# Kernel optimization log

Hardware: AMD Instinct MI355X
Metric: run time of the kernel (lower is better)

## Reference

```python
import jax, jax.numpy as jnp
import numpy as np

# Config constants (match init_kwargs)
D_MODEL = 1024
N_EXPERTS = 8
EXPERT_SCALE = 2          # experts per base group -> n_base_groups = 4
N_FEAT = 16
BANK_DIM = 32
RAW_FEAT = N_FEAT * BANK_DIM   # 512
PROJ_DIM = 256
R_HIDDEN = 256
E_HIDDEN = 256
TOP_K = 2
TEMP = 1.0
LN_EPS = 1e-5


def _layernorm(x, g, b):
    mu = jnp.mean(x, axis=-1, keepdims=True)
    var = jnp.mean((x - mu) ** 2, axis=-1, keepdims=True)
    return (x - mu) * jax.lax.rsqrt(var + LN_EPS) * g + b


def _softmax_top_k(logits, k):
    # keep top-k logits, mask rest to -inf, softmax
    topv = jax.lax.top_k(logits, k)[0]
    thresh = topv[..., -1:]
    masked = jnp.where(logits >= thresh, logits, -jnp.inf)
    return jax.nn.softmax(masked, axis=-1)


def setup_inputs() -> dict:
    key = jax.random.key(0)
    ks = jax.random.split(key, 24)
    B, S = 4, 2048
    s = 0.02
    inp = {
        "hidden": jax.random.normal(ks[0], (B, S, D_MODEL), jnp.float32),
        "feat": jax.random.normal(ks[1], (B, S, N_FEAT), jnp.float32),
        "feat_bank": jax.random.normal(ks[2], (B, S, N_FEAT, BANK_DIM), jnp.float32),
        "item_seq_len": jax.random.randint(ks[3], (B,), 1, S + 1, jnp.int64),
        # pre-LN
        "ln_g": jnp.ones((D_MODEL,), jnp.float32),
        "ln_b": jnp.zeros((D_MODEL,), jnp.float32),
        # router feature projector (2 layers: Linear -> GELU -> Linear)
        "fp_w1": jax.random.normal(ks[4], (RAW_FEAT, PROJ_DIM), jnp.float32) * s,
        "fp_b1": jnp.zeros((PROJ_DIM,), jnp.float32),
        "fp_w2": jax.random.normal(ks[5], (PROJ_DIM, PROJ_DIM), jnp.float32) * s,
        "fp_b2": jnp.zeros((PROJ_DIM,), jnp.float32),
        # learned router MLP: d_in = d_model + proj_dim
        "r_w1": jax.random.normal(ks[6], (D_MODEL + PROJ_DIM, R_HIDDEN), jnp.float32) * s,
        "r_b1": jnp.zeros((R_HIDDEN,), jnp.float32),
        "r_w2": jax.random.normal(ks[7], (R_HIDDEN, N_EXPERTS), jnp.float32) * s,
        "r_b2": jnp.zeros((N_EXPERTS,), jnp.float32),
        # rule router (linear on raw stage features)
        "rr_w": jax.random.normal(ks[8], (N_FEAT, N_EXPERTS), jnp.float32) * s,
        "rr_b": jnp.zeros((N_EXPERTS,), jnp.float32),
        # per-expert FFN
        "e_w1": jax.random.normal(ks[9], (N_EXPERTS, D_MODEL, E_HIDDEN), jnp.float32) * s,
        "e_b1": jnp.zeros((N_EXPERTS, E_HIDDEN), jnp.float32),
        "e_w2": jax.random.normal(ks[10], (N_EXPERTS, E_HIDDEN, D_MODEL), jnp.float32) * s,
        "e_b2": jnp.zeros((N_EXPERTS, D_MODEL), jnp.float32),
        "alpha": jnp.ones((), jnp.float32),
    }
    return inp


def reference(hidden, feat, feat_bank, item_seq_len, ln_g, ln_b,
              fp_w1, fp_b1, fp_w2, fp_b2,
              r_w1, r_b1, r_w2, r_b2,
              rr_w, rr_b,
              e_w1, e_b1, e_w2, e_b2, alpha):
    B, S, D = hidden.shape
    h_norm = _layernorm(hidden, ln_g, ln_b)  # [B,S,D]

    # router feature path: flatten bank, 2-layer GELU projector
    bank_flat = feat_bank.reshape(B, S, RAW_FEAT)
    proj = jnp.dot(jax.nn.gelu(jnp.dot(bank_flat, fp_w1) + fp_b1), fp_w2) + fp_b2  # [B,S,P]

    # token-mode router input: concat hidden + projected features
    router_input = jnp.concatenate([h_norm, proj], axis=-1)
    rule_logits = jnp.dot(feat, rr_w) + rr_b  # rule router on raw stage features

    raw_logits = jnp.dot(jax.nn.gelu(jnp.dot(router_input, r_w1) + r_b1), r_w2) + r_b2
    scaled_logits = raw_logits / max(TEMP, 1e-6)
    gate_weights = _softmax_top_k(scaled_logits, TOP_K)           # [B,S,E]
    rule_target_logits = rule_logits / max(TEMP, 1e-6)

    # expert group: per-expert 2-layer GELU FFN on h_norm
    h1 = jax.nn.gelu(jnp.einsum('bsd,edh->bseh', h_norm, e_w1) + e_b1)
    expert_out = jnp.einsum('bseh,ehd->bsed', h1, e_w2) + e_b2    # [B,S,E,D]

    stage_out = jnp.einsum('bse,bsed->bsd', gate_weights, expert_out)
    next_hidden = hidden + alpha * stage_out

    # _aggregate_group_weights: expert_group_idx = arange(E)//EXPERT_SCALE is
    # contiguous, so gather+sum per group == reshape+sum over the scale axis
    n_groups = N_EXPERTS // EXPERT_SCALE
    group_weights = gate_weights.reshape(B, S, n_groups, EXPERT_SCALE).sum(-1)

    return (next_hidden, stage_out, gate_weights, scaled_logits, group_weights, rule_target_logits)
```

## Files before the change

### kernel.cpp

```cpp
#include <hip/hip_runtime.h>
#include <stdint.h>


typedef unsigned short u16;
using bf16x8 = __attribute__((ext_vector_type(8))) short;
using f32x4  = __attribute__((ext_vector_type(4))) float;

__device__ __forceinline__ float gelu_tanh(float x) {
  float x3 = x * x * x;
  float t = tanhf(0.7978845608028654f * (x + 0.044715f * x3));
  return 0.5f * x * (1.0f + t);
}

__device__ __forceinline__ u16 f2bf(float f) {
  uint32_t u = __float_as_uint(f);
  u = u + 0x7fffu + ((u >> 16) & 1u);
  return (u16)(u >> 16);
}
__device__ __forceinline__ float b2f(u16 h) {
  return __uint_as_float(((uint32_t)h) << 16);
}

__device__ __forceinline__ void gll16(const void* g, void* l) {
  __builtin_amdgcn_global_load_lds(
      (const __attribute__((address_space(1))) void*)g,
      (__attribute__((address_space(3))) void*)l, 16, 0, 0);
}

__global__ __launch_bounds__(256) void split_bank_kernel(const float* __restrict__ x,
    u16* __restrict__ hi, u16* __restrict__ lo) {
  int i4 = blockIdx.x * 256 + threadIdx.x;
  float4 v = ((const float4*)x)[i4];
  ushort4 h, l;
  h.x = f2bf(v.x); l.x = f2bf(v.x - b2f(h.x));
  h.y = f2bf(v.y); l.y = f2bf(v.y - b2f(h.y));
  h.z = f2bf(v.z); l.z = f2bf(v.z - b2f(h.z));
  h.w = f2bf(v.w); l.w = f2bf(v.w - b2f(h.w));
  ((ushort4*)hi)[i4] = h;
  ((ushort4*)lo)[i4] = l;
}

__global__ __launch_bounds__(256) void prep_w_kernel(
    const float* __restrict__ fp_w1, const float* __restrict__ fp_w2,
    const float* __restrict__ r_w1, const float* __restrict__ e_w2,
    u16* __restrict__ w1h, u16* __restrict__ w1l,
    u16* __restrict__ w2h, u16* __restrict__ w2l,
    u16* __restrict__ rwh, u16* __restrict__ rwl,
    u16* __restrict__ ew2t) {
  int idx = blockIdx.x * 256 + threadIdx.x;
  if (idx < 131072) {
    int n = idx >> 9, k = idx & 511;
    float v = fp_w1[k * 256 + n];
    u16 h = f2bf(v); w1h[idx] = h; w1l[idx] = f2bf(v - b2f(h));
  } else if (idx < 196608) {
    int j = idx - 131072;
    int n = j >> 8, k = j & 255;
    float v = fp_w2[k * 256 + n];
    u16 h = f2bf(v); w2h[j] = h; w2l[j] = f2bf(v - b2f(h));
  } else if (idx < 524288) {
    int j = idx - 196608;
    int n = j / 1280, k = j - n * 1280;
    float v = r_w1[k * 256 + n];
    u16 h = f2bf(v); rwh[j] = h; rwl[j] = f2bf(v - b2f(h));
  } else {
    int j = idx - 524288;
    int d = j >> 11, q = j & 2047;
    ew2t[j] = f2bf(e_w2[q * 1024 + d]);
  }
}

__global__ __launch_bounds__(256) void prep_w1t_kernel(const float* __restrict__ ew1,
                                                       u16* __restrict__ w1t) {
  int idx = blockIdx.x * 256 + threadIdx.x;
  int k = idx & 1023, n = idx >> 10;
  int e = n >> 8, h = n & 255;
  w1t[idx] = f2bf(ew1[(e << 18) + (k << 8) + h]);
}

__global__ __launch_bounds__(256) void ln_kernel(const float* __restrict__ hidden,
    const float* __restrict__ ln_g, const float* __restrict__ ln_b,
    const float* __restrict__ feat, const float* __restrict__ rr_w,
    const float* __restrict__ rr_b,
    u16* __restrict__ h_hi, u16* __restrict__ h_lo, float* __restrict__ rule) {
  int t = blockIdx.x;
  int tid = threadIdx.x;
  float4 v = ((const float4*)(hidden + (size_t)t * 1024))[tid];
  float s = v.x + v.y + v.z + v.w;
#pragma unroll
  for (int o = 32; o > 0; o >>= 1) s += __shfl_down(s, o);
  __shared__ float red[4];
  __shared__ float stats[2];
  int wid = tid >> 6, lane = tid & 63;
  if (lane == 0) red[wid] = s;
  __syncthreads();
  if (tid == 0) stats[0] = (red[0] + red[1] + red[2] + red[3]) * (1.0f / 1024.0f);
  __syncthreads();
  float mu = stats[0];
  float dx = v.x - mu, dy = v.y - mu, dz = v.z - mu, dw = v.w - mu;
  float q = dx * dx + dy * dy + dz * dz + dw * dw;
#pragma unroll
  for (int o = 32; o > 0; o >>= 1) q += __shfl_down(q, o);
  if (lane == 0) red[wid] = q;
  __syncthreads();
  if (tid == 0) {
    float var = (red[0] + red[1] + red[2] + red[3]) * (1.0f / 1024.0f) + 1e-5f;
    float r = rsqrtf(var);
    r = r * (1.5f - 0.5f * var * r * r);
    stats[1] = r;
  }
  __syncthreads();
  float r = stats[1];
  float4 g = ((const float4*)ln_g)[tid];
  float4 b = ((const float4*)ln_b)[tid];
  float4 o;
  o.x = dx * r * g.x + b.x;
  o.y = dy * r * g.y + b.y;
  o.z = dz * r * g.z + b.z;
  o.w = dw * r * g.w + b.w;
  ushort4 hv, lv;
  hv.x = f2bf(o.x); lv.x = f2bf(o.x - b2f(hv.x));
  hv.y = f2bf(o.y); lv.y = f2bf(o.y - b2f(hv.y));
  hv.z = f2bf(o.z); lv.z = f2bf(o.z - b2f(hv.z));
  hv.w = f2bf(o.w); lv.w = f2bf(o.w - b2f(hv.w));
  ((ushort4*)(h_hi + (size_t)t * 1024))[tid] = hv;
  ((ushort4*)(h_lo + (size_t)t * 1024))[tid] = lv;
  if (tid < 8) {
    float acc = rr_b[tid];
#pragma unroll
    for (int f = 0; f < 16; f++) acc += feat[t * 16 + f] * rr_w[f * 8 + tid];
    rule[t * 8 + tid] = acc;
  }
}

__global__ __launch_bounds__(256) void gemm3_kernel(
    const u16* __restrict__ Ah, const u16* __restrict__ Al, int lda,
    int kchunk, int nz1,
    const u16* __restrict__ A2h, const u16* __restrict__ A2l, int lda2,
    int klen2, int bkoff2,
    const u16* __restrict__ Bth, const u16* __restrict__ Btl, int Kb,
    float* __restrict__ parts) {
  __shared__ u16 Ash[128 * 32];
  __shared__ u16 Asl[128 * 32];
  __shared__ u16 Bsh[128 * 32];
  __shared__ u16 Bsl[128 * 32];
  int tid = threadIdx.x;
  int z = blockIdx.z;
  const u16 *pAh, *pAl;
  int lda_, akoff, bkoff, klen;
  if (z < nz1) {
    pAh = Ah; pAl = Al; lda_ = lda; akoff = z * kchunk; bkoff = akoff; klen = kchunk;
  } else {
    pAh = A2h; pAl = A2l; lda_ = lda2; akoff = 0; bkoff = bkoff2; klen = klen2;
  }
  int row0 = blockIdx.y * 128, col0 = blockIdx.x * 128;
  int wave = tid >> 6, lane = tid & 63;
  int wr = (wave >> 1) * 64, wc = (wave & 1) * 64;
  int l16 = lane & 15, qd = lane >> 4;
  f32x4 acc[4][4];
#pragma unroll
  for (int i = 0; i < 4; i++)
#pragma unroll
    for (int j = 0; j < 4; j++) acc[i][j] = 0.0f;

  int r0 = tid >> 2, kc = tid & 3;
  const u16* gAh0 = pAh + (size_t)(row0 + r0) * lda_ + akoff + kc * 8;
  const u16* gAh1 = gAh0 + (size_t)64 * lda_;
  const u16* gAl0 = pAl + (size_t)(row0 + r0) * lda_ + akoff + kc * 8;
  const u16* gAl1 = gAl0 + (size_t)64 * lda_;
  const u16* gBh0 = Bth + (size_t)(col0 + r0) * Kb + bkoff + kc * 8;
  const u16* gBh1 = gBh0 + (size_t)64 * Kb;
  const u16* gBl0 = Btl + (size_t)(col0 + r0) * Kb + bkoff + kc * 8;
  const u16* gBl1 = gBl0 + (size_t)64 * Kb;
  u16* dAh = Ash + tid * 8;
  u16* dAl = Asl + tid * 8;
  u16* dBh = Bsh + tid * 8;
  u16* dBl = Bsl + tid * 8;

  for (int k0 = 0; k0 < klen; k0 += 32) {
    __syncthreads();
    gll16(gAh0 + k0, dAh);
    gll16(gAh1 + k0, dAh + 2048);
    gll16(gAl0 + k0, dAl);
    gll16(gAl1 + k0, dAl + 2048);
    gll16(gBh0 + k0, dBh);
    gll16(gBh1 + k0, dBh + 2048);
    gll16(gBl0 + k0, dBl);
    gll16(gBl1 + k0, dBl + 2048);
    __syncthreads();
    bf16x8 afh[4], afl[4], bfh[4], bfl[4];
#pragma unroll
    for (int i = 0; i < 4; i++) {
      afh[i] = *((const bf16x8*)(Ash + (wr + i * 16 + l16) * 32 + qd * 8));
      afl[i] = *((const bf16x8*)(Asl + (wr + i * 16 + l16) * 32 + qd * 8));
      bfh[i] = *((const bf16x8*)(Bsh + (wc + i * 16 + l16) * 32 + qd * 8));
      bfl[i] = *((const bf16x8*)(Bsl + (wc + i * 16 + l16) * 32 + qd * 8));
    }
#pragma unroll
    for (int i = 0; i < 4; i++)
#pragma unroll
      for (int j = 0; j < 4; j++) {
        acc[i][j] = __builtin_amdgcn_mfma_f32_16x16x32_bf16(afh[i], bfh[j], acc[i][j], 0, 0, 0);
        acc[i][j] = __builtin_amdgcn_mfma_f32_16x16x32_bf16(afl[i], bfh[j], acc[i][j], 0, 0, 0);
        acc[i][j] = __builtin_amdgcn_mfma_f32_16x16x32_bf16(afh[i], bfl[j], acc[i][j], 0, 0, 0);
      }
  }

  float* pz = parts + (size_t)z * 2097152;
#pragma unroll
  for (int i = 0; i < 4; i++)
#pragma unroll
    for (int j = 0; j < 4; j++) {
      int cl = wc + j * 16 + l16;
#pragma unroll
      for (int rr = 0; rr < 4; rr++) {
        int rl = wr + i * 16 + qd * 4 + rr;
        pz[(size_t)(row0 + rl) * 256 + col0 + cl] = acc[i][j][rr];
      }
    }
}

__global__ __launch_bounds__(256) void epi_bf_kernel(const float* __restrict__ parts,
    int nz, const float* __restrict__ bias, int do_gelu,
    u16* __restrict__ hi, u16* __restrict__ lo) {
  int i4 = blockIdx.x * 256 + threadIdx.x;
  float4 s = ((const float4*)parts)[i4];
  for (int zz = 1; zz < nz; zz++) {
    float4 p = ((const float4*)parts)[(size_t)zz * 524288 + i4];
    s.x += p.x; s.y += p.y; s.z += p.z; s.w += p.w;
  }
  float4 bv = ((const float4*)bias)[i4 & 63];
  s.x += bv.x; s.y += bv.y; s.z += bv.z; s.w += bv.w;
  if (do_gelu) {
    s.x = gelu_tanh(s.x); s.y = gelu_tanh(s.y);
    s.z = gelu_tanh(s.z); s.w = gelu_tanh(s.w);
  }
  ushort4 h, l;
  h.x = f2bf(s.x); l.x = f2bf(s.x - b2f(h.x));
  h.y = f2bf(s.y); l.y = f2bf(s.y - b2f(h.y));
  h.z = f2bf(s.z); l.z = f2bf(s.z - b2f(h.z));
  h.w = f2bf(s.w); l.w = f2bf(s.w - b2f(h.w));
  ((ushort4*)hi)[i4] = h;
  ((ushort4*)lo)[i4] = l;
}

__global__ __launch_bounds__(256) void epi_f32_kernel(const float* __restrict__ parts,
    int nz, const float* __restrict__ bias, float* __restrict__ out) {
  int i4 = blockIdx.x * 256 + threadIdx.x;
  float4 s = ((const float4*)parts)[i4];
  for (int zz = 1; zz < nz; zz++) {
    float4 p = ((const float4*)parts)[(size_t)zz * 524288 + i4];
    s.x += p.x; s.y += p.y; s.z += p.z; s.w += p.w;
  }
  float4 bv = ((const float4*)bias)[i4 & 63];
  s.x = gelu_tanh(s.x + bv.x);
  s.y = gelu_tanh(s.y + bv.y);
  s.z = gelu_tanh(s.z + bv.z);
  s.w = gelu_tanh(s.w + bv.w);
  ((float4*)out)[i4] = s;
}

__global__ __launch_bounds__(256) void gate_kernel(const float* __restrict__ r1,
    const float* __restrict__ r_w2, const float* __restrict__ r_b2,
    float* __restrict__ gates, float* __restrict__ slog, float* __restrict__ gw) {
  __shared__ float w2s[2048];
  __shared__ float r1s[32][260];
  __shared__ float lg[32][8];
  int tid = threadIdx.x;
  int t0 = blockIdx.x * 32;
  for (int i = tid; i < 2048; i += 256) w2s[i] = r_w2[i];
  for (int i = tid; i < 32 * 256; i += 256) {
    int tt = i >> 8, k = i & 255;
    r1s[tt][k] = r1[(size_t)(t0 + tt) * 256 + k];
  }
  __syncthreads();
  int tl = tid >> 3, e = tid & 7;
  float acc = r_b2[e];
  for (int k = 0; k < 256; k++) acc += r1s[tl][k] * w2s[k * 8 + e];
  lg[tl][e] = acc;
  __syncthreads();
  if (tid < 32) {
    int t = t0 + tid;
    float l[8];
#pragma unroll
    for (int i = 0; i < 8; i++) l[i] = lg[tid][i];
    float m1 = -1e30f, m2 = -1e30f;
#pragma unroll
    for (int i = 0; i < 8; i++) {
      float v = l[i];
      if (v > m1) { m2 = m1; m1 = v; }
      else if (v > m2) m2 = v;
    }
    float w[8];
    float se = 0.0f;
#pragma unroll
    for (int i = 0; i < 8; i++) {
      float ex = (l[i] >= m2) ? expf(l[i] - m1) : 0.0f;
      w[i] = ex;
      se += ex;
    }
    float inv = 1.0f / se;
#pragma unroll
    for (int i = 0; i < 8; i++) {
      gates[(size_t)t * 8 + i] = w[i] * inv;
      slog[(size_t)t * 8 + i] = l[i];
    }
#pragma unroll
    for (int gi = 0; gi < 4; gi++)
      gw[(size_t)t * 4 + gi] = (w[2 * gi] + w[2 * gi + 1]) * inv;
  }
}

template <int MODE>
__global__ __launch_bounds__(256) void mfma_gemm(const u16* __restrict__ A,
    const u16* __restrict__ Bt, int N, int K,
    const float* __restrict__ bias, const float* __restrict__ gates,
    u16* __restrict__ outb, const float* __restrict__ hidden,
    const float* __restrict__ alpha_p, float* __restrict__ stage,
    float* __restrict__ next) {
  __shared__ u16 As[128 * 32];
  __shared__ u16 Bs[128 * 32];
  __shared__ float gs[128 * 8];
  __shared__ float b2s[8 * 128];
  int tid = threadIdx.x;
  int row0 = blockIdx.y * 128, col0 = blockIdx.x * 128;
  int wave = tid >> 6, lane = tid & 63;
  int wr = (wave >> 1) * 64, wc = (wave & 1) * 64;
  int l16 = lane & 15, qd = lane >> 4;
  f32x4 acc[4][4];
#pragma unroll
  for (int i = 0; i < 4; i++)
#pragma unroll
    for (int j = 0; j < 4; j++) acc[i][j] = 0.0f;

  int r0 = tid >> 2, kc = tid & 3;
  const u16* Ap0 = A + (size_t)(row0 + r0) * K + kc * 8;
  const u16* Ap1 = Ap0 + (size_t)64 * K;
  const u16* Bp0 = Bt + (size_t)(col0 + r0) * K + kc * 8;
  const u16* Bp1 = Bp0 + (size_t)64 * K;
  u16* dA = As + tid * 8;
  u16* dB = Bs + tid * 8;

  for (int k0 = 0; k0 < K; k0 += 32) {
    __syncthreads();
    gll16(Ap0 + k0, dA);
    gll16(Ap1 + k0, dA + 2048);
    gll16(Bp0 + k0, dB);
    gll16(Bp1 + k0, dB + 2048);
    __syncthreads();
    bf16x8 af[4], bfr[4];
#pragma unroll
    for (int i = 0; i < 4; i++) {
      af[i]  = *((const bf16x8*)(As + (wr + i * 16 + l16) * 32 + qd * 8));
      bfr[i] = *((const bf16x8*)(Bs + (wc + i * 16 + l16) * 32 + qd * 8));
    }
#pragma unroll
    for (int i = 0; i < 4; i++)
#pragma unroll
      for (int j = 0; j < 4; j++)
        acc[i][j] = __builtin_amdgcn_mfma_f32_16x16x32_bf16(af[i], bfr[j], acc[i][j], 0, 0, 0);
  }

  for (int i = tid; i < 1024; i += 256)
    gs[i] = gates[(size_t)(row0 + (i >> 3)) * 8 + (i & 7)];
  if (MODE == 1) {
    for (int i = tid; i < 1024; i += 256)
      b2s[i] = bias[(size_t)(i >> 7) * 1024 + col0 + (i & 127)];
  }
  __syncthreads();

  if (MODE == 0) {
#pragma unroll
    for (int i = 0; i < 4; i++) {
#pragma unroll
      for (int j = 0; j < 4; j++) {
        int cl = wc + j * 16 + l16;
        int col = col0 + cl;
        float bcol = bias[col];
        int e = col >> 8;
#pragma unroll
        for (int rr = 0; rr < 4; rr++) {
          int rl = wr + i * 16 + qd * 4 + rr;
          int row = row0 + rl;
          float v = acc[i][j][rr] + bcol;
          v = gelu_tanh(v) * gs[rl * 8 + e];
          outb[(size_t)row * N + col] = f2bf(v);
        }
      }
    }
  } else {
    float al = alpha_p[0];
#pragma unroll
    for (int i = 0; i < 4; i++) {
#pragma unroll
      for (int j = 0; j < 4; j++) {
        int cl = wc + j * 16 + l16;
        int col = col0 + cl;
#pragma unroll
        for (int rr = 0; rr < 4; rr++) {
          int rl = wr + i * 16 + qd * 4 + rr;
          int row = row0 + rl;
          float sb = 0.0f;
#pragma unroll
          for (int e = 0; e < 8; e++) sb += gs[rl * 8 + e] * b2s[e * 128 + cl];
          float v = acc[i][j][rr] + sb;
          size_t o = (size_t)row * N + col;
          stage[o] = v;
          next[o] = hidden[o] + al * v;
        }
      }
    }
  }
}

extern "C" void kernel_launch(void* const* d_in, const int* in_sizes, int n_in,
                              void* d_out, int out_size, void* d_ws, size_t ws_size,
                              hipStream_t stream) {
  const float* hidden    = (const float*)d_in[0];
  const float* feat      = (const float*)d_in[1];
  const float* feat_bank = (const float*)d_in[2];
  const float* ln_g  = (const float*)d_in[4];
  const float* ln_b  = (const float*)d_in[5];
  const float* fp_w1 = (const float*)d_in[6];
  const float* fp_b1 = (const float*)d_in[7];
  const float* fp_w2 = (const float*)d_in[8];
  const float* fp_b2 = (const float*)d_in[9];
  const float* r_w1  = (const float*)d_in[10];
  const float* r_b1  = (const float*)d_in[11];
  const float* r_w2  = (const float*)d_in[12];
  const float* r_b2  = (const float*)d_in[13];
  const float* rr_w  = (const float*)d_in[14];
  const float* rr_b  = (const float*)d_in[15];
  const float* e_w1  = (const float*)d_in[16];
  const float* e_b1  = (const float*)d_in[17];
  const float* e_w2  = (const float*)d_in[18];
  const float* e_b2  = (const float*)d_in[19];
  const float* alpha = (const float*)d_in[20];

  char* ob = (char*)d_out;
  float* next  = (float*)ob;
  float* stage = (float*)(ob + 33554432);
  float* gates = (float*)(ob + 67108864);
  float* slog  = gates + 65536;
  float* gw    = slog + 65536;
  float* rule  = gw + 32768;

  u16* bank_hi  = (u16*)(ob);
  u16* bank_lo  = (u16*)(ob + 8388608);
  u16* fpw1t_hi = (u16*)(ob + 16777216);
  u16* fpw1t_lo = (u16*)(ob + 17039360);
  u16* mid_hi   = (u16*)(ob + 16777216);
  u16* mid_lo   = (u16*)(ob + 20971520);
  u16* fpw2t_hi = (u16*)(ob + 25165824);
  u16* fpw2t_lo = (u16*)(ob + 25296896);
  u16* proj_hi  = (u16*)(ob + 25165824);
  u16* proj_lo  = (u16*)(ob + 29360128);
  u16* w1t      = (u16*)(ob);
  char* sb = ob + 33554432;
  float* parts  = (float*)sb;
  u16* rw1t_hi  = (u16*)(sb + 25165824);
  u16* rw1t_lo  = (u16*)(sb + 25821184);
  float* r1     = (float*)(sb + 25165824);

  char* ws = (char*)d_ws;
  u16* apr  = (u16*)ws;
  u16* h_hi = (u16*)(ws + 33554432);
  u16* h_lo = (u16*)(ws + 50331648);
  u16* w2t  = (u16*)(ws + 67108864);

  split_bank_kernel<<<4096, 256, 0, stream>>>(feat_bank, bank_hi, bank_lo);
  prep_w_kernel<<<10240, 256, 0, stream>>>(fp_w1, fp_w2, r_w1, e_w2,
      fpw1t_hi, fpw1t_lo, fpw2t_hi, fpw2t_lo, rw1t_hi, rw1t_lo, w2t);
  ln_kernel<<<8192, 256, 0, stream>>>(hidden, ln_g, ln_b, feat, rr_w, rr_b,
                                      h_hi, h_lo, rule);
  gemm3_kernel<<<dim3(2, 64, 2), 256, 0, stream>>>(
      bank_hi, bank_lo, 512, 256, 2,
      bank_hi, bank_lo, 512, 0, 0,
      fpw1t_hi, fpw1t_lo, 512, parts);
  epi_bf_kernel<<<2048, 256, 0, stream>>>(parts, 2, fp_b1, 1, mid_hi, mid_lo);
  prep_w1t_kernel<<<8192, 256, 0, stream>>>(e_w1, w1t);
  gemm3_kernel<<<dim3(2, 64, 2), 256, 0, stream>>>(
      mid_hi, mid_lo, 256, 128, 2,
      mid_hi, mid_lo, 256, 0, 0,
      fpw2t_hi, fpw2t_lo, 256, parts);
  epi_bf_kernel<<<2048, 256, 0, stream>>>(parts, 2, fp_b2, 0, proj_hi, proj_lo);
  gemm3_kernel<<<dim3(2, 64, 3), 256, 0, stream>>>(
      h_hi, h_lo, 1024, 512, 2,
      proj_hi, proj_lo, 256, 256, 1024,
      rw1t_hi, rw1t_lo, 1280, parts);
  epi_f32_kernel<<<2048, 256, 0, stream>>>(parts, 3, r_b1, r1);
  gate_kernel<<<256, 256, 0, stream>>>(r1, r_w2, r_b2, gates, slog, gw);
  mfma_gemm<0><<<dim3(16, 64), 256, 0, stream>>>(h_hi, w1t, 2048, 1024, e_b1, gates,
      apr, nullptr, nullptr, nullptr, nullptr);
  mfma_gemm<1><<<dim3(8, 64), 256, 0, stream>>>(apr, w2t, 1024, 2048, e_b2, gates,
      nullptr, hidden, alpha, stage, next);
}
```

Measured before the change: 409.6 us.

## Route tokens sparsely to top-2 experts and fold projector layer into router weights

```diff
diff --git a/kernel.cpp b/kernel.cpp
--- a/kernel.cpp
+++ b/kernel.cpp
@@ -5,13 +5,28 @@
 typedef unsigned short u16;
 using bf16x8 = __attribute__((ext_vector_type(8))) short;
 using f32x4  = __attribute__((ext_vector_type(4))) float;
+
+#define WS_HHI 0u
+#define WS_HLO 16777216u
+#define WS_PB2 33554432u
+#define WS_IDX 67108864u
+#define IX_TOK    0u
+#define IX_GPOS   262144u
+#define IX_SELE   524288u
+#define IX_SELP   589824u
+#define IX_SELG   655360u
+#define IX_ROW    720896u
+#define IX_TILEE  786432u
+#define IX_TILEL  790528u
+#define IX_TILES  794624u
+#define IX_TILEC  798720u
+#define IX_META   802816u
 
 __device__ __forceinline__ float gelu_tanh(float x) {
   float x3 = x * x * x;
   float t = tanhf(0.7978845608028654f * (x + 0.044715f * x3));
   return 0.5f * x * (1.0f + t);
 }
-
 __device__ __forceinline__ u16 f2bf(float f) {
   uint32_t u = __float_as_uint(f);
   u = u + 0x7fffu + ((u >> 16) & 1u);
@@ -20,7 +35,6 @@
 __device__ __forceinline__ float b2f(u16 h) {
   return __uint_as_float(((uint32_t)h) << 16);
 }
-
 __device__ __forceinline__ void gll16(const void* g, void* l) {
   __builtin_amdgcn_global_load_lds(
       (const __attribute__((address_space(1))) void*)g,
@@ -40,41 +54,55 @@
   ((ushort4*)lo)[i4] = l;
 }
 
-__global__ __launch_bounds__(256) void prep_w_kernel(
-    const float* __restrict__ fp_w1, const float* __restrict__ fp_w2,
-    const float* __restrict__ r_w1, const float* __restrict__ e_w2,
+__global__ __launch_bounds__(256) void wprime_kernel(const float* __restrict__ fp_w2,
+    const float* __restrict__ r_w1, const float* __restrict__ fp_b2,
+    const float* __restrict__ r_b1, float* __restrict__ wp, float* __restrict__ bp) {
+  __shared__ float row[256];
+  int i = blockIdx.x, n = threadIdx.x;
+  if (i < 256) {
+    row[n] = fp_w2[i * 256 + n];
+    __syncthreads();
+    float acc = 0.0f;
+    for (int j = 0; j < 256; j++) acc += row[j] * r_w1[(size_t)(1024 + j) * 256 + n];
+    wp[i * 256 + n] = acc;
+  } else {
+    row[n] = fp_b2[n];
+    __syncthreads();
+    float acc = r_b1[n];
+    for (int j = 0; j < 256; j++) acc += row[j] * r_w1[(size_t)(1024 + j) * 256 + n];
+    bp[n] = acc;
+  }
+}
+
+__global__ __launch_bounds__(256) void prep_main_kernel(
+    const float* __restrict__ fp_w1, const float* __restrict__ e_w1,
+    const float* __restrict__ e_w2,
     u16* __restrict__ w1h, u16* __restrict__ w1l,
-    u16* __restrict__ w2h, u16* __restrict__ w2l,
-    u16* __restrict__ rwh, u16* __restrict__ rwl,
-    u16* __restrict__ ew2t) {
+    u16* __restrict__ w1t, u16* __restrict__ w2te) {
   int idx = blockIdx.x * 256 + threadIdx.x;
   if (idx < 131072) {
     int n = idx >> 9, k = idx & 511;
     float v = fp_w1[k * 256 + n];
     u16 h = f2bf(v); w1h[idx] = h; w1l[idx] = f2bf(v - b2f(h));
-  } else if (idx < 196608) {
+  } else if (idx < 131072 + 2097152) {
     int j = idx - 131072;
-    int n = j >> 8, k = j & 255;
-    float v = fp_w2[k * 256 + n];
-    u16 h = f2bf(v); w2h[j] = h; w2l[j] = f2bf(v - b2f(h));
-  } else if (idx < 524288) {
-    int j = idx - 196608;
-    int n = j / 1280, k = j - n * 1280;
-    float v = r_w1[k * 256 + n];
-    u16 h = f2bf(v); rwh[j] = h; rwl[j] = f2bf(v - b2f(h));
+    int k = j & 1023, n = j >> 10;
+    int e = n >> 8, h = n & 255;
+    w1t[j] = f2bf(e_w1[(e << 18) + (k << 8) + h]);
   } else {
-    int j = idx - 524288;
-    int d = j >> 11, q = j & 2047;
-    ew2t[j] = f2bf(e_w2[q * 1024 + d]);
-  }
-}
-
-__global__ __launch_bounds__(256) void prep_w1t_kernel(const float* __restrict__ ew1,
-                                                       u16* __restrict__ w1t) {
+    int j = idx - 131072 - 2097152;
+    int h = j & 255, row = j >> 8;
+    int d = row & 1023, e = row >> 10;
+    w2te[j] = f2bf(e_w2[(e << 18) + (h << 10) + d]);
+  }
+}
+
+__global__ __launch_bounds__(256) void prep_rw_kernel(const float* __restrict__ r_w1,
+    const float* __restrict__ wp, u16* __restrict__ rh, u16* __restrict__ rl) {
   int idx = blockIdx.x * 256 + threadIdx.x;
-  int k = idx & 1023, n = idx >> 10;
-  int e = n >> 8, h = n & 255;
-  w1t[idx] = f2bf(ew1[(e << 18) + (k << 8) + h]);
+  int n = idx / 1280, k = idx - n * 1280;
+  float v = (k < 1024) ? r_w1[(size_t)k * 256 + n] : wp[(k - 1024) * 256 + n];
+  u16 h = f2bf(v); rh[idx] = h; rl[idx] = f2bf(v - b2f(h));
 }
 
 __global__ __launch_bounds__(256) void ln_kernel(const float* __restrict__ hidden,
@@ -261,7 +289,10 @@
 
 __global__ __launch_bounds__(256) void gate_kernel(const float* __restrict__ r1,
     const float* __restrict__ r_w2, const float* __restrict__ r_b2,
-    float* __restrict__ gates, float* __restrict__ slog, float* __restrict__ gw) {
+    float* __restrict__ gates, float* __restrict__ slog, float* __restrict__ gw,
+    int* __restrict__ tok, float* __restrict__ gpos,
+    int* __restrict__ selE, int* __restrict__ selP, float* __restrict__ selG,
+    int* __restrict__ meta) {
   __shared__ float w2s[2048];
   __shared__ float r1s[32][260];
   __shared__ float lg[32][8];
@@ -284,11 +315,12 @@
 #pragma unroll
     for (int i = 0; i < 8; i++) l[i] = lg[tid][i];
     float m1 = -1e30f, m2 = -1e30f;
+    int i1 = 0, i2 = 0;
 #pragma unroll
     for (int i = 0; i < 8; i++) {
       float v = l[i];
-      if (v > m1) { m2 = m1; m1 = v; }
-      else if (v > m2) m2 = v;
+      if (v > m1) { m2 = m1; i2 = i1; m1 = v; i1 = i; }
+      else if (v > m2) { m2 = v; i2 = i; }
     }
     float w[8];
     float se = 0.0f;
@@ -307,22 +339,60 @@
 #pragma unroll
     for (int gi = 0; gi < 4; gi++)
       gw[(size_t)t * 4 + gi] = (w[2 * gi] + w[2 * gi + 1]) * inv;
-  }
-}
-
-template <int MODE>
-__global__ __launch_bounds__(256) void mfma_gemm(const u16* __restrict__ A,
-    const u16* __restrict__ Bt, int N, int K,
-    const float* __restrict__ bias, const float* __restrict__ gates,
-    u16* __restrict__ outb, const float* __restrict__ hidden,
-    const float* __restrict__ alpha_p, float* __restrict__ stage,
-    float* __restrict__ next) {
+    float g1 = w[i1] * inv, g2 = w[i2] * inv;
+    int p1 = atomicAdd(&meta[i1], 1);
+    tok[i1 * 8192 + p1] = t; gpos[i1 * 8192 + p1] = g1;
+    selE[t * 2] = i1; selP[t * 2] = p1; selG[t * 2] = g1;
+    int p2 = atomicAdd(&meta[i2], 1);
+    tok[i2 * 8192 + p2] = t; gpos[i2 * 8192 + p2] = g2;
+    selE[t * 2 + 1] = i2; selP[t * 2 + 1] = p2; selG[t * 2 + 1] = g2;
+  }
+}
+
+__global__ __launch_bounds__(256) void tilemap_kernel(int* __restrict__ meta,
+    int* __restrict__ tileE, int* __restrict__ tileL, int* __restrict__ tileS,
+    int* __restrict__ tileC, const int* __restrict__ selE,
+    const int* __restrict__ selP, int* __restrict__ rowsel) {
+  __shared__ int sbase[8];
+  int tid = threadIdx.x;
+  if (tid == 0) {
+    int b = 0, nt = 0;
+    for (int e = 0; e < 8; e++) {
+      sbase[e] = b;
+      int c = meta[e];
+      for (int off = 0; off < c; off += 128) {
+        tileE[nt] = e; tileL[nt] = off; tileS[nt] = b + off;
+        tileC[nt] = (c - off < 128) ? (c - off) : 128;
+        nt++;
+      }
+      b += c;
+    }
+    meta[16] = nt;
+  }
+  __syncthreads();
+  for (int i = tid; i < 16384; i += 256)
+    rowsel[i] = sbase[selE[i]] + selP[i];
+}
+
+__global__ __launch_bounds__(256) void gexp1_kernel(const u16* __restrict__ A,
+    const u16* __restrict__ w1t, const float* __restrict__ e_b1,
+    const int* __restrict__ tok, const float* __restrict__ gpos,
+    const int* __restrict__ tileE, const int* __restrict__ tileL,
+    const int* __restrict__ tileS, const int* __restrict__ tileC,
+    const int* __restrict__ meta, u16* __restrict__ pb1) {
+  int ty = blockIdx.y;
+  if (ty >= meta[16]) return;
+  int e = tileE[ty], loc = tileL[ty], pstart = tileS[ty], pcnt = tileC[ty];
+  if (pcnt <= 0) return;
   __shared__ u16 As[128 * 32];
   __shared__ u16 Bs[128 * 32];
-  __shared__ float gs[128 * 8];
-  __shared__ float b2s[8 * 128];
+  __shared__ float gsl[128];
   int tid = threadIdx.x;
-  int row0 = blockIdx.y * 128, col0 = blockIdx.x * 128;
+  int col0 = blockIdx.x * 128;
+  if (tid < 128) {
+    int rr = (tid < pcnt) ? tid : (pcnt - 1);
+    gsl[tid] = gpos[e * 8192 + loc + rr];
+  }
   int wave = tid >> 6, lane = tid & 63;
   int wr = (wave >> 1) * 64, wc = (wave & 1) * 64;
   int l16 = lane & 15, qd = lane >> 4;
@@ -333,14 +403,18 @@
     for (int j = 0; j < 4; j++) acc[i][j] = 0.0f;
 
   int r0 = tid >> 2, kc = tid & 3;
-  const u16* Ap0 = A + (size_t)(row0 + r0) * K + kc * 8;
-  const u16* Ap1 = Ap0 + (size_t)64 * K;
-  const u16* Bp0 = Bt + (size_t)(col0 + r0) * K + kc * 8;
-  const u16* Bp1 = Bp0 + (size_t)64 * K;
+  int ra = (r0 < pcnt) ? r0 : (pcnt - 1);
+  int rb = (r0 + 64 < pcnt) ? (r0 + 64) : (pcnt - 1);
+  int ta = tok[e * 8192 + loc + ra];
+  int tb = tok[e * 8192 + loc + rb];
+  const u16* Ap0 = A + (size_t)ta * 1024 + kc * 8;
+  const u16* Ap1 = A + (size_t)tb * 1024 + kc * 8;
+  const u16* Bp0 = w1t + (size_t)(e * 256 + col0 + r0) * 1024 + kc * 8;
+  const u16* Bp1 = Bp0 + (size_t)64 * 1024;
   u16* dA = As + tid * 8;
   u16* dB = Bs + tid * 8;
 
-  for (int k0 = 0; k0 < K; k0 += 32) {
+  for (int k0 = 0; k0 < 1024; k0 += 32) {
     __syncthreads();
     gll16(Ap0 + k0, dA);
     gll16(Ap1 + k0, dA + 2048);
@@ -360,56 +434,116 @@
         acc[i][j] = __builtin_amdgcn_mfma_f32_16x16x32_bf16(af[i], bfr[j], acc[i][j], 0, 0, 0);
   }
 
-  for (int i = tid; i < 1024; i += 256)
-    gs[i] = gates[(size_t)(row0 + (i >> 3)) * 8 + (i & 7)];
-  if (MODE == 1) {
-    for (int i = tid; i < 1024; i += 256)
-      b2s[i] = bias[(size_t)(i >> 7) * 1024 + col0 + (i & 127)];
-  }
-  __syncthreads();
-
-  if (MODE == 0) {
-#pragma unroll
-    for (int i = 0; i < 4; i++) {
-#pragma unroll
-      for (int j = 0; j < 4; j++) {
-        int cl = wc + j * 16 + l16;
-        int col = col0 + cl;
-        float bcol = bias[col];
-        int e = col >> 8;
-#pragma unroll
-        for (int rr = 0; rr < 4; rr++) {
-          int rl = wr + i * 16 + qd * 4 + rr;
-          int row = row0 + rl;
-          float v = acc[i][j][rr] + bcol;
-          v = gelu_tanh(v) * gs[rl * 8 + e];
-          outb[(size_t)row * N + col] = f2bf(v);
+#pragma unroll
+  for (int i = 0; i < 4; i++)
+#pragma unroll
+    for (int j = 0; j < 4; j++) {
+      int cl = wc + j * 16 + l16;
+      int col = col0 + cl;
+      float bcol = e_b1[e * 256 + col];
+#pragma unroll
+      for (int rr = 0; rr < 4; rr++) {
+        int rl = wr + i * 16 + qd * 4 + rr;
+        if (rl < pcnt) {
+          float v = gelu_tanh(acc[i][j][rr] + bcol) * gsl[rl];
+          pb1[(size_t)(pstart + rl) * 256 + col] = f2bf(v);
         }
       }
     }
-  } else {
-    float al = alpha_p[0];
+}
+
+__global__ __launch_bounds__(256) void gexp2_kernel(const u16* __restrict__ pb1,
+    const u16* __restrict__ w2te,
+    const int* __restrict__ tileE, const int* __restrict__ tileS,
+    const int* __restrict__ tileC, const int* __restrict__ meta,
+    u16* __restrict__ pb2) {
+  int ty = blockIdx.y;
+  if (ty >= meta[16]) return;
+  int e = tileE[ty], pstart = tileS[ty], pcnt = tileC[ty];
+  if (pcnt <= 0) return;
+  __shared__ u16 As[128 * 32];
+  __shared__ u16 Bs[128 * 32];
+  int tid = threadIdx.x;
+  int col0 = blockIdx.x * 128;
+  int wave = tid >> 6, lane = tid & 63;
+  int wr = (wave >> 1) * 64, wc = (wave & 1) * 64;
+  int l16 = lane & 15, qd = lane >> 4;
+  f32x4 acc[4][4];
+#pragma unroll
+  for (int i = 0; i < 4; i++)
+#pragma unroll
+    for (int j = 0; j < 4; j++) acc[i][j] = 0.0f;
+
+  int r0 = tid >> 2, kc = tid & 3;
+  int ra = (r0 < pcnt) ? r0 : (pcnt - 1);
+  int rb = (r0 + 64 < pcnt) ? (r0 + 64) : (pcnt - 1);
+  const u16* Ap0 = pb1 + (size_t)(pstart + ra) * 256 + kc * 8;
+  const u16* Ap1 = pb1 + (size_t)(pstart + rb) * 256 + kc * 8;
+  const u16* Bp0 = w2te + (size_t)(e * 1024 + col0 + r0) * 256 + kc * 8;
+  const u16* Bp1 = Bp0 + (size_t)64 * 256;
+  u16* dA = As + tid * 8;
+  u16* dB = Bs + tid * 8;
+
+  for (int k0 = 0; k0 < 256; k0 += 32) {
+    __syncthreads();
+    gll16(Ap0 + k0, dA);
+    gll16(Ap1 + k0, dA + 2048);
+    gll16(Bp0 + k0, dB);
+    gll16(Bp1 + k0, dB + 2048);
+    __syncthreads();
+    bf16x8 af[4], bfr[4];
 #pragma unroll
     for (int i = 0; i < 4; i++) {
-#pragma unroll
-      for (int j = 0; j < 4; j++) {
-        int cl = wc + j * 16 + l16;
-        int col = col0 + cl;
-#pragma unroll
-        for (int rr = 0; rr < 4; rr++) {
-          int rl = wr + i * 16 + qd * 4 + rr;
-          int row = row0 + rl;
-          float sb = 0.0f;
-#pragma unroll
-          for (int e = 0; e < 8; e++) sb += gs[rl * 8 + e] * b2s[e * 128 + cl];
-          float v = acc[i][j][rr] + sb;
-          size_t o = (size_t)row * N + col;
-          stage[o] = v;
-          next[o] = hidden[o] + al * v;
-        }
+      af[i]  = *((const bf16x8*)(As + (wr + i * 16 + l16) * 32 + qd * 8));
+      bfr[i] = *((const bf16x8*)(Bs + (wc + i * 16 + l16) * 32 + qd * 8));
+    }
+#pragma unroll
+    for (int i = 0; i < 4; i++)
+#pragma unroll
+      for (int j = 0; j < 4; j++)
+        acc[i][j] = __builtin_amdgcn_mfma_f32_16x16x32_bf16(af[i], bfr[j], acc[i][j], 0, 0, 0);
+  }
+
+#pragma unroll
+  for (int i = 0; i < 4; i++)
+#pragma unroll
+    for (int j = 0; j < 4; j++) {
+      int cl = wc + j * 16 + l16;
+#pragma unroll
+      for (int rr = 0; rr < 4; rr++) {
+        int rl = wr + i * 16 + qd * 4 + rr;
+        if (rl < pcnt)
+          pb2[(size_t)(pstart + rl) * 1024 + col0 + cl] = f2bf(acc[i][j][rr]);
       }
     }
-  }
+}
+
+__global__ __launch_bounds__(256) void combine_kernel(const u16* __restrict__ pb2,
+    const int* __restrict__ rowsel, const int* __restrict__ selE,
+    const float* __restrict__ selG, const float* __restrict__ e_b2,
+    const float* __restrict__ hidden, const float* __restrict__ alpha_p,
+    float* __restrict__ stage, float* __restrict__ next) {
+  int t = blockIdx.x;
+  int c = threadIdx.x * 4;
+  int rA = rowsel[t * 2], rB = rowsel[t * 2 + 1];
+  int eA = selE[t * 2], eB = selE[t * 2 + 1];
+  float gA = selG[t * 2], gB = selG[t * 2 + 1];
+  float al = alpha_p[0];
+  ushort4 pa = *((const ushort4*)(pb2 + (size_t)rA * 1024 + c));
+  ushort4 pb = *((const ushort4*)(pb2 + (size_t)rB * 1024 + c));
+  float4 ba = *((const float4*)(e_b2 + (size_t)eA * 1024 + c));
+  float4 bb = *((const float4*)(e_b2 + (size_t)eB * 1024 + c));
+  float4 h = *((const float4*)(hidden + (size_t)t * 1024 + c));
+  float4 v;
+  v.x = b2f(pa.x) + b2f(pb.x) + gA * ba.x + gB * bb.x;
+  v.y = b2f(pa.y) + b2f(pb.y) + gA * ba.y + gB * bb.y;
+  v.z = b2f(pa.z) + b2f(pb.z) + gA * ba.z + gB * bb.z;
+  v.w = b2f(pa.w) + b2f(pb.w) + gA * ba.w + gB * bb.w;
+  *((float4*)(stage + (size_t)t * 1024 + c)) = v;
+  float4 n;
+  n.x = h.x + al * v.x; n.y = h.y + al * v.y;
+  n.z = h.z + al * v.z; n.w = h.w + al * v.w;
+  *((float4*)(next + (size_t)t * 1024 + c)) = n;
 }
 
 extern "C" void kernel_launch(void* const* d_in, const int* in_sizes, int n_in,
@@ -444,32 +578,48 @@
   float* gw    = slog + 65536;
   float* rule  = gw + 32768;
 
-  u16* bank_hi  = (u16*)(ob);
+  u16* bank_hi  = (u16*)ob;
   u16* bank_lo  = (u16*)(ob + 8388608);
+  float* r1     = (float*)ob;
   u16* fpw1t_hi = (u16*)(ob + 16777216);
   u16* fpw1t_lo = (u16*)(ob + 17039360);
-  u16* mid_hi   = (u16*)(ob + 16777216);
-  u16* mid_lo   = (u16*)(ob + 20971520);
-  u16* fpw2t_hi = (u16*)(ob + 25165824);
-  u16* fpw2t_lo = (u16*)(ob + 25296896);
-  u16* proj_hi  = (u16*)(ob + 25165824);
-  u16* proj_lo  = (u16*)(ob + 29360128);
-  u16* w1t      = (u16*)(ob);
+  float* wp     = (float*)(ob + 17301504);
+  float* bp     = (float*)(ob + 17563648);
+  u16* rw1t_hi  = (u16*)(ob + 17825792);
+  u16* rw1t_lo  = (u16*)(ob + 18481152);
+  u16* mid_hi   = (u16*)(ob + 19136512);
+  u16* mid_lo   = (u16*)(ob + 23330816);
+
   char* sb = ob + 33554432;
-  float* parts  = (float*)sb;
-  u16* rw1t_hi  = (u16*)(sb + 25165824);
-  u16* rw1t_lo  = (u16*)(sb + 25821184);
-  float* r1     = (float*)(sb + 25165824);
+  float* parts = (float*)sb;
+  u16* pb1     = (u16*)sb;
+  u16* w1t     = (u16*)(sb + 25165824);
+  u16* w2te    = (u16*)(sb + 29360128);
 
   char* ws = (char*)d_ws;
-  u16* apr  = (u16*)ws;
-  u16* h_hi = (u16*)(ws + 33554432);
-  u16* h_lo = (u16*)(ws + 50331648);
-  u16* w2t  = (u16*)(ws + 67108864);
+  u16* h_hi = (u16*)(ws + WS_HHI);
+  u16* h_lo = (u16*)(ws + WS_HLO);
+  u16* pb2  = (u16*)(ws + WS_PB2);
+  char* ix  = ws + WS_IDX;
+  int*   tok    = (int*)(ix + IX_TOK);
+  float* gpos   = (float*)(ix + IX_GPOS);
+  int*   selE   = (int*)(ix + IX_SELE);
+  int*   selP   = (int*)(ix + IX_SELP);
+  float* selG   = (float*)(ix + IX_SELG);
+  int*   rowsel = (int*)(ix + IX_ROW);
+  int*   tileE  = (int*)(ix + IX_TILEE);
+  int*   tileL  = (int*)(ix + IX_TILEL);
+  int*   tileS  = (int*)(ix + IX_TILES);
+  int*   tileC  = (int*)(ix + IX_TILEC);
+  int*   meta   = (int*)(ix + IX_META);
+
+  hipMemsetAsync(ix + IX_TILEE, 0, 32768, stream);
 
   split_bank_kernel<<<4096, 256, 0, stream>>>(feat_bank, bank_hi, bank_lo);
-  prep_w_kernel<<<10240, 256, 0, stream>>>(fp_w1, fp_w2, r_w1, e_w2,
-      fpw1t_hi, fpw1t_lo, fpw2t_hi, fpw2t_lo, rw1t_hi, rw1t_lo, w2t);
+  wprime_kernel<<<257, 256, 0, stream>>>(fp_w2, r_w1, fp_b2, r_b1, wp, bp);
+  prep_main_kernel<<<16896, 256, 0, stream>>>(fp_w1, e_w1, e_w2,
+      fpw1t_hi, fpw1t_lo, w1t, w2te);
+  prep_rw_kernel<<<1280, 256, 0, stream>>>(r_w1, wp, rw1t_hi, rw1t_lo);
   ln_kernel<<<8192, 256, 0, stream>>>(hidden, ln_g, ln_b, feat, rr_w, rr_b,
                                       h_hi, h_lo, rule);
   gemm3_kernel<<<dim3(2, 64, 2), 256, 0, stream>>>(
@@ -477,20 +627,19 @@
       bank_hi, bank_lo, 512, 0, 0,
       fpw1t_hi, fpw1t_lo, 512, parts);
   epi_bf_kernel<<<2048, 256, 0, stream>>>(parts, 2, fp_b1, 1, mid_hi, mid_lo);
-  prep_w1t_kernel<<<8192, 256, 0, stream>>>(e_w1, w1t);
-  gemm3_kernel<<<dim3(2, 64, 2), 256, 0, stream>>>(
-      mid_hi, mid_lo, 256, 128, 2,
-      mid_hi, mid_lo, 256, 0, 0,
-      fpw2t_hi, fpw2t_lo, 256, parts);
-  epi_bf_kernel<<<2048, 256, 0, stream>>>(parts, 2, fp_b2, 0, proj_hi, proj_lo);
   gemm3_kernel<<<dim3(2, 64, 3), 256, 0, stream>>>(
       h_hi, h_lo, 1024, 512, 2,
-      proj_hi, proj_lo, 256, 256, 1024,
+      mid_hi, mid_lo, 256, 256, 1024,
       rw1t_hi, rw1t_lo, 1280, parts);
-  epi_f32_kernel<<<2048, 256, 0, stream>>>(parts, 3, r_b1, r1);
-  gate_kernel<<<256, 256, 0, stream>>>(r1, r_w2, r_b2, gates, slog, gw);
-  mfma_gemm<0><<<dim3(16, 64), 256, 0, stream>>>(h_hi, w1t, 2048, 1024, e_b1, gates,
-      apr, nullptr, nullptr, nullptr, nullptr);
-  mfma_gemm<1><<<dim3(8, 64), 256, 0, stream>>>(apr, w2t, 1024, 2048, e_b2, gates,
-      nullptr, hidden, alpha, stage, next);
-}
+  epi_f32_kernel<<<2048, 256, 0, stream>>>(parts, 3, bp, r1);
+  gate_kernel<<<256, 256, 0, stream>>>(r1, r_w2, r_b2, gates, slog, gw,
+      tok, gpos, selE, selP, selG, meta);
+  tilemap_kernel<<<1, 256, 0, stream>>>(meta, tileE, tileL, tileS, tileC,
+      selE, selP, rowsel);
+  gexp1_kernel<<<dim3(2, 136), 256, 0, stream>>>(h_hi, w1t, e_b1, tok, gpos,
+      tileE, tileL, tileS, tileC, meta, pb1);
+  gexp2_kernel<<<dim3(8, 136), 256, 0, stream>>>(pb1, w2te, tileE, tileS, tileC,
+      meta, pb2);
+  combine_kernel<<<8192, 256, 0, stream>>>(pb2, rowsel, selE, selG, e_b2,
+      hidden, alpha, stage, next);
+}
```

Measured after the change: 428.2 us. 1.05x slower.
